# Performance work log

Hardware: AMD Instinct MI355X
Metric: run time of the kernel (lower is better)

## Reference

```python
import jax, jax.numpy as jnp
import numpy as np

B, IC2, N, K = 8, 128, 2048, 32   # x: [B, 2*in_channels, N, k]
C, G = 64, 8                       # out_channels, groups
CPG = C // G                       # channels per group
EPS_BN = 1e-5


def conv1x1(x, w, b=None):
    # 1x1 conv over [B, Cin, N, K] with weight [Cout, Cin]
    y = jnp.einsum('oc,bcnk->bonk', w, x)
    if b is not None:
        y = y + b[None, :, None, None]
    return y


def bn(x, g, beta, m, v):
    # inference-mode BatchNorm2d
    scale = g / jnp.sqrt(v + EPS_BN)
    return x * scale[None, :, None, None] + (beta - m * scale)[None, :, None, None]


def lrelu(x):
    return jax.nn.leaky_relu(x, 0.2)


def setup_inputs() -> dict:
    key = jax.random.key(0)
    ks = jax.random.split(key, 32)
    d = {}
    d['x'] = jax.random.normal(ks[0], (B, IC2, N, K), jnp.float32)
    d['rel_pos'] = jax.random.normal(ks[1], (B, 3, N, K), jnp.float32)
    # pos_net
    d['pos_w1'] = jax.random.normal(ks[2], (C, 3), jnp.float32) * 0.1
    d['pos_bn_g'] = jax.random.uniform(ks[3], (C,), jnp.float32, 0.5, 1.5)
    d['pos_bn_b'] = jax.random.normal(ks[4], (C,), jnp.float32) * 0.1
    d['pos_bn_m'] = jax.random.normal(ks[5], (C,), jnp.float32) * 0.1
    d['pos_bn_v'] = jax.random.uniform(ks[6], (C,), jnp.float32, 0.5, 1.5)
    d['pos_w2'] = jax.random.normal(ks[7], (C, C), jnp.float32) * 0.1
    d['pos_b2'] = jax.random.normal(ks[8], (C,), jnp.float32) * 0.1
    # pe_proj
    d['pe_w'] = jax.random.normal(ks[9], (G, C), jnp.float32) * 0.1
    d['pe_b'] = jax.random.normal(ks[10], (G,), jnp.float32) * 0.1
    # trans (Conv+BN+LeakyReLU)
    d['trans_w'] = jax.random.normal(ks[11], (C, IC2), jnp.float32) * 0.1
    d['trans_bn_g'] = jax.random.uniform(ks[12], (C,), jnp.float32, 0.5, 1.5)
    d['trans_bn_b'] = jax.random.normal(ks[13], (C,), jnp.float32) * 0.1
    d['trans_bn_m'] = jax.random.normal(ks[14], (C,), jnp.float32) * 0.1
    d['trans_bn_v'] = jax.random.uniform(ks[15], (C,), jnp.float32, 0.5, 1.5)
    # gate_net (hidden 16)
    d['gate_w1'] = jax.random.normal(ks[16], (16, IC2), jnp.float32) * 0.1
    d['gate_bn_g'] = jax.random.uniform(ks[17], (16,), jnp.float32, 0.5, 1.5)
    d['gate_bn_b'] = jax.random.normal(ks[18], (16,), jnp.float32) * 0.1
    d['gate_bn_m'] = jax.random.normal(ks[19], (16,), jnp.float32) * 0.1
    d['gate_bn_v'] = jax.random.uniform(ks[20], (16,), jnp.float32, 0.5, 1.5)
    d['gate_w2'] = jax.random.normal(ks[21], (1, 16), jnp.float32) * 0.1
    d['gate_b2'] = jnp.full((1,), 2.0, jnp.float32)  # init.constant_(bias, 2.0)
    # attn_net (hidden C//4 = 16)
    d['attn_w1'] = jax.random.normal(ks[22], (C // 4, IC2), jnp.float32) * 0.1
    d['attn_bn_g'] = jax.random.uniform(ks[23], (C // 4,), jnp.float32, 0.5, 1.5)
    d['attn_bn_b'] = jax.random.normal(ks[24], (C // 4,), jnp.float32) * 0.1
    d['attn_bn_m'] = jax.random.normal(ks[25], (C // 4,), jnp.float32) * 0.1
    d['attn_bn_v'] = jax.random.uniform(ks[26], (C // 4,), jnp.float32, 0.5, 1.5)
    d['attn_w2'] = jax.random.normal(ks[27], (G, C // 4), jnp.float32) * 0.1
    d['attn_b2'] = jax.random.normal(ks[28], (G,), jnp.float32) * 0.1
    return d


def reference(x, rel_pos, pos_w1, pos_bn_g, pos_bn_b, pos_bn_m, pos_bn_v, pos_w2, pos_b2,
              pe_w, pe_b, trans_w, trans_bn_g, trans_bn_b, trans_bn_m, trans_bn_v,
              gate_w1, gate_bn_g, gate_bn_b, gate_bn_m, gate_bn_v, gate_w2, gate_b2,
              attn_w1, attn_bn_g, attn_bn_b, attn_bn_m, attn_bn_v, attn_w2, attn_b2):
    # pos_net: conv -> BN -> LeakyReLU -> conv(bias)
    pos_enc = conv1x1(lrelu(bn(conv1x1(rel_pos, pos_w1), pos_bn_g, pos_bn_b, pos_bn_m, pos_bn_v)),
                      pos_w2, pos_b2)                                    # [B,C,N,K]
    # trans: conv -> BN -> LeakyReLU, plus positional encoding
    trans_feat = lrelu(bn(conv1x1(x, trans_w), trans_bn_g, trans_bn_b, trans_bn_m, trans_bn_v)) + pos_enc
    # gate_net (dropout=identity in eval): -> sigmoid gate [B,1,N,K]
    gate_h = lrelu(bn(conv1x1(x, gate_w1), gate_bn_g, gate_bn_b, gate_bn_m, gate_bn_v))
    gate_map = jax.nn.sigmoid(conv1x1(gate_h, gate_w2, gate_b2))
    # attn_net -> grouped logits [B,G,N,K]
    attn_h = lrelu(bn(conv1x1(x, attn_w1), attn_bn_g, attn_bn_b, attn_bn_m, attn_bn_v))
    attn_logits = conv1x1(attn_h, attn_w2, attn_b2)
    attn_logits = attn_logits + conv1x1(pos_enc, pe_w, pe_b)             # pe_proj
    attn_logits = attn_logits + jnp.log(gate_map + 1e-6)                 # full mode: log-combine gate
    attn_w = jax.nn.softmax(attn_logits, axis=-1)                        # softmax over neighbors k
    attn_w_exp = jnp.repeat(attn_w, CPG, axis=1)                         # repeat_interleave -> [B,C,N,K]
    out_attn = jnp.sum(trans_feat * attn_w_exp, axis=-1)                 # [B,C,N]
    out_max = jnp.max(trans_feat * gate_map, axis=-1)                    # [B,C,N]
    return out_attn + out_max
```

## Files before the change

kernel.cpp:

```cpp
#include <hip/hip_runtime.h>


typedef __attribute__((ext_vector_type(8))) short bf16x8;
typedef __attribute__((ext_vector_type(4))) float f32x4;

#define EPS_BN 1e-5f

__device__ __forceinline__ unsigned pk2(float a, float b){
  unsigned ua = __float_as_uint(a) + 0x8000u;
  unsigned ub = __float_as_uint(b) + 0x8000u;
  return __builtin_amdgcn_perm(ub, ua, 0x07060302);
}
__device__ __forceinline__ short f2bf(float a){
  unsigned u = __float_as_uint(a);
  u += 0x7FFFu + ((u >> 16) & 1u);
  return (short)(u >> 16);
}
__device__ __forceinline__ float lrelu(float v){ return fmaxf(v, 0.2f*v); }

__device__ __forceinline__ void st8(short* dst, float4 a, float4 b){
  *(uint2*)(dst)     = make_uint2(pk2(a.x,a.y), pk2(a.z,a.w));
  *(uint2*)(dst + 4) = make_uint2(pk2(b.x,b.y), pk2(b.z,b.w));
}
__device__ __forceinline__ bf16x8 ld8(const short* p){
  union { bf16x8 v; uint2 q[2]; } w;
  w.q[0] = *(const uint2*)(p);
  w.q[1] = *(const uint2*)(p + 4);
  return w.v;
}

template<int N>
__device__ __forceinline__ float ror16(float x){
  return __int_as_float(__builtin_amdgcn_mov_dpp(__float_as_int(x), 0x120+N, 0xF, 0xF, false));
}
__device__ __forceinline__ float rsum16(float v){
  v += ror16<1>(v); v += ror16<2>(v); v += ror16<4>(v); v += ror16<8>(v); return v;
}
__device__ __forceinline__ float rmax16(float v){
  v = fmaxf(v, ror16<1>(v)); v = fmaxf(v, ror16<2>(v));
  v = fmaxf(v, ror16<4>(v)); v = fmaxf(v, ror16<8>(v)); return v;
}

#define MFMA16(a,b,c) __builtin_amdgcn_mfma_f32_16x16x32_bf16((a),(b),(c),0,0,0)

__global__ __launch_bounds__(256, 2)
void gsl_fused(const float* __restrict__ x,       const float* __restrict__ rel_pos,
               const float* __restrict__ pos_w1,  const float* __restrict__ pos_g,
               const float* __restrict__ pos_bb,  const float* __restrict__ pos_m,
               const float* __restrict__ pos_v,   const float* __restrict__ pos_w2,
               const float* __restrict__ pos_b2,  const float* __restrict__ pe_w,
               const float* __restrict__ pe_b,    const float* __restrict__ trans_w,
               const float* __restrict__ tr_g,    const float* __restrict__ tr_bb,
               const float* __restrict__ tr_m,    const float* __restrict__ tr_v,
               const float* __restrict__ gate_w1, const float* __restrict__ ga_g,
               const float* __restrict__ ga_bb,   const float* __restrict__ ga_m,
               const float* __restrict__ ga_v,    const float* __restrict__ gate_w2,
               const float* __restrict__ gate_b2, const float* __restrict__ attn_w1,
               const float* __restrict__ at_g,    const float* __restrict__ at_bb,
               const float* __restrict__ at_m,    const float* __restrict__ at_v,
               const float* __restrict__ attn_w2, const float* __restrict__ attn_b2,
               float* __restrict__ out)
{
  __shared__ __align__(16) char smem[70784];
  short* xbuf  = (short*)smem;
  short* wmain = (short*)(smem + 33792);
  short* wpos2 = (short*)(smem + 59136);
  float* trQ  = (float*)(smem + 68928);
  float* p1T  = (float*)(smem + 69952);
  float* gaT  = (float*)(smem + 70464);
  float* atT  = (float*)(smem + 70592);
  float* peBt = (float*)(smem + 70720);

  const int tid = threadIdx.x;
  const int wv  = tid >> 6;
  const int l   = tid & 63;
  const int l15 = l & 15, g4 = l >> 4;
  const int bid = blockIdx.x;
  const int b    = bid >> 6;
  const int nblk = (bid & 63) << 5;

  if (tid < 192){
    int r = tid >> 1, c0 = (tid & 1) * 64;
    const float* src = (r < 64) ? (trans_w + r*128)
                     : (r < 80) ? (gate_w1 + (r-64)*128)
                                : (attn_w1 + (r-80)*128);
    src += c0;
    short* dst = wmain + r*132 + c0;
    #pragma unroll
    for (int j = 0; j < 8; ++j)
      st8(dst + 8*j, *(const float4*)(src + 8*j), *(const float4*)(src + 8*j + 4));
  } else {
    int r = tid - 192;
    const float* src = pos_w2 + r*64;
    short* dst = wpos2 + r*68;
    #pragma unroll
    for (int j = 0; j < 8; ++j)
      st8(dst + 8*j, *(const float4*)(src + 8*j), *(const float4*)(src + 8*j + 4));
  }
  if (tid < 64){
    float s = tr_g[tid] * rsqrtf(tr_v[tid] + EPS_BN);
    *(float4*)(trQ + 4*tid) = make_float4(s, tr_bb[tid] - tr_m[tid]*s, pos_b2[tid], 0.f);
    float s2 = pos_g[tid] * rsqrtf(pos_v[tid] + EPS_BN);
    p1T[2*tid] = s2; p1T[2*tid+1] = pos_bb[tid] - pos_m[tid]*s2;
  } else if (tid < 80){
    int c = tid - 64;
    float s = ga_g[c] * rsqrtf(ga_v[c] + EPS_BN);
    gaT[2*c] = s; gaT[2*c+1] = ga_bb[c] - ga_m[c]*s;
  } else if (tid < 96){
    int c = tid - 80;
    float s = at_g[c] * rsqrtf(at_v[c] + EPS_BN);
    atT[2*c] = s; atT[2*c+1] = at_bb[c] - at_m[c]*s;
  } else if (tid < 112){
    int r2 = tid - 96;
    float v = 0.f;
    if (r2 < 8){
      v = pe_b[r2];
      for (int c = 0; c < 64; ++c) v += pe_w[r2*64 + c] * pos_b2[c];
    }
    peBt[r2] = v;
  }
  {
    int o = 2*tid, r = o >> 6, j = o & 63;
    float c0 = 0.f, c1 = 0.f;
    for (int c = 0; c < 64; ++c){
      float a = pe_w[r*64 + c];
      c0 += a * pos_w2[c*64 + j];
      c1 += a * pos_w2[c*64 + j + 1];
    }
    *(unsigned*)(wpos2 + (64 + r)*68 + j) = pk2(c0, c1);
  }

  uint2 pw1p[4];
  #pragma unroll
  for (int m2 = 0; m2 < 4; ++m2){
    uint2 t = make_uint2(0u, 0u);
    if (g4 == 0){
      const float* rp = pos_w1 + (16*m2 + l15)*3;
      t.x = pk2(rp[0], rp[1]);
      t.y = pk2(rp[2], 0.f);
    }
    pw1p[m2] = t;
  }
  bf16x8 gaf;
  {
    bf16x8 t = {0,0,0,0,0,0,0,0};
    #pragma unroll
    for (int j = 0; j < 8; ++j){
      int k = 8*g4 + j;
      float v2 = 0.f;
      if (l15 < 8)       { if (k >= 16) v2 = attn_w2[l15*16 + (k-16)]; }
      else if (l15 == 8) { if (k < 16)  v2 = gate_w2[k]; }
      t[j] = f2bf(v2);
    }
    gaf = t;
  }
  const float gb2v = gate_b2[0];

  __syncthreads();

  float lcr[4];
  #pragma unroll
  for (int r = 0; r < 4; ++r){
    int row = 4*g4 + r;
    lcr[r] = peBt[row] + ((row < 8) ? attn_b2[row] : 0.f);
  }

  const int col0 = 32*wv + l15, col1 = col0 + 16;
  const int lc0 = l15, lc1 = l15 + 16;
  const int lq = l & 7, ld = l >> 3;
  const int colb = 32*wv + 4*lq;
  char*  slice = smem + wv*8448;
  short* h1b   = (short*)slice;
  short* gab   = (short*)(slice + 4352);
  const float* xp0 = x + (((long)(b*128 + 8*ld)) << 16) + colb;
  const float* rpb = rel_pos + (((long)(3*b)) << 16);
  float* outb = out + (((long)(b*64)) << 11) + nblk + wv;

  f32x4 fa[8], fb[8];
  float rc[6] = {0.f,0.f,0.f,0.f,0.f,0.f};
  {
    const long sb0 = (long)nblk * 32;
    #pragma unroll
    for (int j = 0; j < 8; ++j) fa[j] = *(const f32x4*)(xp0 + sb0 + (((long)j) << 16));
    #pragma unroll
    for (int j = 0; j < 8; ++j) fb[j] = *(const f32x4*)(xp0 + sb0 + (((long)(64+j)) << 16));
    if (g4 == 0){
      long sg = sb0 + col0;
      rc[0] = rpb[sg];          rc[1] = rpb[sg + 65536];      rc[2] = rpb[sg + 131072];
      rc[3] = rpb[sg + 16];     rc[4] = rpb[sg + 65536 + 16]; rc[5] = rpb[sg + 131072 + 16];
    }
  }

  for (int it = 0; it < 8; ++it){
    const long sbase = (long)nblk*32 + 128*it;

    #pragma unroll
    for (int i2 = 0; i2 < 4; ++i2){
      short* dst = xbuf + (colb+i2)*132 + 8*ld;
      *(uint2*)(dst)      = make_uint2(pk2(fa[0][i2],fa[1][i2]), pk2(fa[2][i2],fa[3][i2]));
      *(uint2*)(dst + 4)  = make_uint2(pk2(fa[4][i2],fa[5][i2]), pk2(fa[6][i2],fa[7][i2]));
      *(uint2*)(dst + 64) = make_uint2(pk2(fb[0][i2],fb[1][i2]), pk2(fb[2][i2],fb[3][i2]));
      *(uint2*)(dst + 68) = make_uint2(pk2(fb[4][i2],fb[5][i2]), pk2(fb[6][i2],fb[7][i2]));
    }

    const long nsb = sbase + 128;
    if (it < 7){
      #pragma unroll
      for (int j = 0; j < 8; ++j) fa[j] = *(const f32x4*)(xp0 + nsb + (((long)j) << 16));
    }

    f32x4 acc[6][2];
    #pragma unroll
    for (int m = 0; m < 6; ++m){
      f32x4 z = {0.f,0.f,0.f,0.f};
      acc[m][0] = z; acc[m][1] = z;
    }
    #pragma unroll
    for (int ks = 0; ks < 4; ++ks){
      bf16x8 b0 = ld8(xbuf + col0*132 + 32*ks + 8*g4);
      bf16x8 b1 = ld8(xbuf + col1*132 + 32*ks + 8*g4);
      #pragma unroll
      for (int m = 0; m < 6; ++m){
        bf16x8 af = ld8(wmain + (16*m + l15)*132 + 32*ks + 8*g4);
        acc[m][0] = MFMA16(af, b0, acc[m][0]);
        acc[m][1] = MFMA16(af, b1, acc[m][1]);
      }
    }

    if (it < 7){
      #pragma unroll
      for (int j = 0; j < 8; ++j) fb[j] = *(const f32x4*)(xp0 + nsb + (((long)(64+j)) << 16));
    }

    {
      bf16x8 rf0 = {0,0,0,0,0,0,0,0}, rf1 = {0,0,0,0,0,0,0,0};
      if (g4 == 0){
        union { bf16x8 v; unsigned u[4]; } t0, t1;
        t0.u[0] = pk2(rc[0], rc[1]); t0.u[1] = pk2(rc[2], 0.f); t0.u[2] = 0u; t0.u[3] = 0u;
        t1.u[0] = pk2(rc[3], rc[4]); t1.u[1] = pk2(rc[5], 0.f); t1.u[2] = 0u; t1.u[3] = 0u;
        rf0 = t0.v; rf1 = t1.v;
      }
      #pragma unroll
      for (int m2 = 0; m2 < 4; ++m2){
        union { bf16x8 v; unsigned u[4]; } aw;
        aw.u[0] = pw1p[m2].x; aw.u[1] = pw1p[m2].y; aw.u[2] = 0u; aw.u[3] = 0u;
        f32x4 z = {0.f,0.f,0.f,0.f};
        f32x4 d0 = MFMA16(aw.v, rf0, z);
        f32x4 d1 = MFMA16(aw.v, rf1, z);
        int cb2 = 16*m2 + 4*g4;
        float2 t0 = *(const float2*)(p1T + 2*(cb2+0));
        float2 t1 = *(const float2*)(p1T + 2*(cb2+1));
        float2 t2 = *(const float2*)(p1T + 2*(cb2+2));
        float2 t3 = *(const float2*)(p1T + 2*(cb2+3));
        float h0 = lrelu(t0.x*d0[0]+t0.y), h1v = lrelu(t1.x*d0[1]+t1.y);
        float h2 = lrelu(t2.x*d0[2]+t2.y), h3 = lrelu(t3.x*d0[3]+t3.y);
        *(uint2*)(h1b + lc0*68 + cb2) = make_uint2(pk2(h0,h1v), pk2(h2,h3));
        h0 = lrelu(t0.x*d1[0]+t0.y); h1v = lrelu(t1.x*d1[1]+t1.y);
        h2 = lrelu(t2.x*d1[2]+t2.y); h3 = lrelu(t3.x*d1[3]+t3.y);
        *(uint2*)(h1b + lc1*68 + cb2) = make_uint2(pk2(h0,h1v), pk2(h2,h3));
      }
    }
    if (g4 == 0 && it < 7){
      long sg = nsb + col0;
      rc[0] = rpb[sg];          rc[1] = rpb[sg + 65536];      rc[2] = rpb[sg + 131072];
      rc[3] = rpb[sg + 16];     rc[4] = rpb[sg + 65536 + 16]; rc[5] = rpb[sg + 131072 + 16];
    }

    #pragma unroll
    for (int m = 0; m < 4; ++m)
      #pragma unroll
      for (int r = 0; r < 4; ++r){
        float4 tq = *(const float4*)(trQ + 4*(16*m + 4*g4 + r));
        acc[m][0][r] = lrelu(tq.x*acc[m][0][r] + tq.y) + tq.z;
        acc[m][1][r] = lrelu(tq.x*acc[m][1][r] + tq.y) + tq.z;
      }

    f32x4 pac4[2];
    {
      f32x4 z = {0.f,0.f,0.f,0.f};
      pac4[0] = z; pac4[1] = z;
    }
    #pragma unroll
    for (int ks = 0; ks < 2; ++ks){
      bf16x8 h0 = ld8(h1b + lc0*68 + 32*ks + 8*g4);
      bf16x8 h1v = ld8(h1b + lc1*68 + 32*ks + 8*g4);
      #pragma unroll
      for (int m2 = 0; m2 < 4; ++m2){
        bf16x8 af = ld8(wpos2 + (16*m2 + l15)*68 + 32*ks + 8*g4);
        acc[m2][0] = MFMA16(af, h0, acc[m2][0]);
        acc[m2][1] = MFMA16(af, h1v, acc[m2][1]);
      }
      bf16x8 af4 = ld8(wpos2 + (64 + l15)*68 + 32*ks + 8*g4);
      pac4[0] = MFMA16(af4, h0, pac4[0]);
      pac4[1] = MFMA16(af4, h1v, pac4[1]);
    }

    {
      int hc = 4*g4;
      float2 g0p = *(const float2*)(gaT + 2*(hc+0));
      float2 g1p = *(const float2*)(gaT + 2*(hc+1));
      float2 g2p = *(const float2*)(gaT + 2*(hc+2));
      float2 g3p = *(const float2*)(gaT + 2*(hc+3));
      float2 a0p = *(const float2*)(atT + 2*(hc+0));
      float2 a1p = *(const float2*)(atT + 2*(hc+1));
      float2 a2p = *(const float2*)(atT + 2*(hc+2));
      float2 a3p = *(const float2*)(atT + 2*(hc+3));
      #pragma unroll
      for (int ct = 0; ct < 2; ++ct){
        int lc = (ct == 0) ? lc0 : lc1;
        float q0 = lrelu(g0p.x*acc[4][ct][0] + g0p.y), q1 = lrelu(g1p.x*acc[4][ct][1] + g1p.y);
        float q2 = lrelu(g2p.x*acc[4][ct][2] + g2p.y), q3 = lrelu(g3p.x*acc[4][ct][3] + g3p.y);
        *(uint2*)(gab + lc*36 + hc) = make_uint2(pk2(q0,q1), pk2(q2,q3));
        float a0 = lrelu(a0p.x*acc[5][ct][0] + a0p.y), a1 = lrelu(a1p.x*acc[5][ct][1] + a1p.y);
        float a2 = lrelu(a2p.x*acc[5][ct][2] + a2p.y), a3 = lrelu(a3p.x*acc[5][ct][3] + a3p.y);
        *(uint2*)(gab + lc*36 + 16 + hc) = make_uint2(pk2(a0,a1), pk2(a2,a3));
      }
    }

    f32x4 gac0 = {0.f,0.f,0.f,0.f}, gac1 = gac0;
    {
      bf16x8 g0 = ld8(gab + lc0*36 + 8*g4);
      bf16x8 g1 = ld8(gab + lc1*36 + 8*g4);
      gac0 = MFMA16(gaf, g0, gac0);
      gac1 = MFMA16(gaf, g1, gac1);
    }

    float gv0 = __shfl(gac0[0], 32 + l15, 64);
    float gv1 = __shfl(gac1[0], 32 + l15, 64);
    float gm0 = 1.f/(1.f + __expf(-(gv0 + gb2v)));
    float gm1 = 1.f/(1.f + __expf(-(gv1 + gb2v)));
    float lg0 = __logf(gm0 + 1e-6f), lg1 = __logf(gm1 + 1e-6f);

    float wg0[4], wg1[4];
    #pragma unroll
    for (int r = 0; r < 4; ++r){
      float t0 = gac0[r] + pac4[0][r] + lcr[r] + lg0;
      float t1 = gac1[r] + pac4[1][r] + lcr[r] + lg1;
      float mx = rmax16(fmaxf(t0, t1));
      float e0 = __expf(t0 - mx), e1 = __expf(t1 - mx);
      float inv = 1.f / rsum16(e0 + e1);
      wg0[r] = e0 * inv; wg1[r] = e1 * inv;
    }
    float wf0[8], wf1[8];
    #pragma unroll
    for (int gg = 0; gg < 8; ++gg){
      int src = 16*(gg >> 2) + l15;
      wf0[gg] = __shfl(wg0[gg & 3], src, 64);
      wf1[gg] = __shfl(wg1[gg & 3], src, 64);
    }
    const bool hi = (g4 >= 2);
    #pragma unroll
    for (int m = 0; m < 4; ++m){
      float w0 = hi ? wf0[2*m+1] : wf0[2*m];
      float w1 = hi ? wf1[2*m+1] : wf1[2*m];
      #pragma unroll
      for (int r = 0; r < 4; ++r){
        float sA = rsum16(acc[m][0][r]*w0 + acc[m][1][r]*w1);
        float sM = rmax16(fmaxf(acc[m][0][r]*gm0, acc[m][1][r]*gm1));
        if (l15 == 0)
          outb[(((long)(16*m + 4*g4 + r)) << 11) + 4*it] = sA + sM;
      }
    }
  }
}

extern "C" void kernel_launch(void* const* d_in, const int* in_sizes, int n_in,
                              void* d_out, int out_size, void* d_ws, size_t ws_size,
                              hipStream_t stream){
  (void)in_sizes; (void)n_in; (void)out_size; (void)d_ws; (void)ws_size;
  gsl_fused<<<dim3(512), dim3(256), 0, stream>>>(
    (const float*)d_in[0],  (const float*)d_in[1],  (const float*)d_in[2],
    (const float*)d_in[3],  (const float*)d_in[4],  (const float*)d_in[5],
    (const float*)d_in[6],  (const float*)d_in[7],  (const float*)d_in[8],
    (const float*)d_in[9],  (const float*)d_in[10], (const float*)d_in[11],
    (const float*)d_in[12], (const float*)d_in[13], (const float*)d_in[14],
    (const float*)d_in[15], (const float*)d_in[16], (const float*)d_in[17],
    (const float*)d_in[18], (const float*)d_in[19], (const float*)d_in[20],
    (const float*)d_in[21], (const float*)d_in[22], (const float*)d_in[23],
    (const float*)d_in[24], (const float*)d_in[25], (const float*)d_in[26],
    (const float*)d_in[27], (const float*)d_in[28], (const float*)d_in[29],
    (float*)d_out);
}
```

Baseline: 75.44 us.

## Hoist pe_w·pos_w2 fold to prep kernel and use transpose-reduce for outputs

Moves the per-block folding of pe_w with pos_w2 and pe_b with pos_b2 into a single-block prep kernel that writes to workspace. The main kernel now only loads those results, which removes a 64-iteration dot-product loop from every block's prologue. The barrier is moved after the first global prefetch so those loads overlap the setup. The epilogue replaces 32 separate 16-lane DPP reductions, each written by one lane, with a butterfly transpose-reduce so every lane ends up owning one output channel and stores it. The cost is an extra kernel launch and a dependency on workspace.

Result: faster. 70.02 us (median of 2 runs) (-7.2%).

```diff
diff --git a/kernel.cpp b/kernel.cpp
--- a/kernel.cpp
+++ b/kernel.cpp
@@ -43,13 +43,30 @@
 
 #define MFMA16(a,b,c) __builtin_amdgcn_mfma_f32_16x16x32_bf16((a),(b),(c),0,0,0)
 
+__global__ void gsl_prep(const float* __restrict__ pos_w2, const float* __restrict__ pe_w,
+                         const float* __restrict__ pe_b,   const float* __restrict__ pos_b2,
+                         float* __restrict__ ws){
+  int t = threadIdx.x;
+  int r = t >> 6, j = t & 63;
+  float s = 0.f;
+  for (int c = 0; c < 64; ++c) s += pe_w[r*64 + c] * pos_w2[c*64 + j];
+  ws[t] = s;
+  if (t < 16){
+    float v = 0.f;
+    if (t < 8){
+      v = pe_b[t];
+      for (int c = 0; c < 64; ++c) v += pe_w[t*64 + c] * pos_b2[c];
+    }
+    ws[512 + t] = v;
+  }
+}
+
 __global__ __launch_bounds__(256, 2)
 void gsl_fused(const float* __restrict__ x,       const float* __restrict__ rel_pos,
                const float* __restrict__ pos_w1,  const float* __restrict__ pos_g,
                const float* __restrict__ pos_bb,  const float* __restrict__ pos_m,
                const float* __restrict__ pos_v,   const float* __restrict__ pos_w2,
-               const float* __restrict__ pos_b2,  const float* __restrict__ pe_w,
-               const float* __restrict__ pe_b,    const float* __restrict__ trans_w,
+               const float* __restrict__ pos_b2,  const float* __restrict__ trans_w,
                const float* __restrict__ tr_g,    const float* __restrict__ tr_bb,
                const float* __restrict__ tr_m,    const float* __restrict__ tr_v,
                const float* __restrict__ gate_w1, const float* __restrict__ ga_g,
@@ -59,7 +76,7 @@
                const float* __restrict__ at_g,    const float* __restrict__ at_bb,
                const float* __restrict__ at_m,    const float* __restrict__ at_v,
                const float* __restrict__ attn_w2, const float* __restrict__ attn_b2,
-               float* __restrict__ out)
+               const float* __restrict__ ws,      float* __restrict__ out)
 {
   __shared__ __align__(16) char smem[70784];
   short* xbuf  = (short*)smem;
@@ -69,7 +86,6 @@
   float* p1T  = (float*)(smem + 69952);
   float* gaT  = (float*)(smem + 70464);
   float* atT  = (float*)(smem + 70592);
-  float* peBt = (float*)(smem + 70720);
 
   const int tid = threadIdx.x;
   const int wv  = tid >> 6;
@@ -95,6 +111,14 @@
     short* dst = wpos2 + r*68;
     #pragma unroll
     for (int j = 0; j < 8; ++j)
+      st8(dst + 8*j, *(const float4*)(src + 8*j), *(const float4*)(src + 8*j + 4));
+  }
+  if (tid < 16){
+    int r = tid >> 1, c0 = (tid & 1) * 32;
+    const float* src = ws + r*64 + c0;
+    short* dst = wpos2 + (64 + r)*68 + c0;
+    #pragma unroll
+    for (int j = 0; j < 4; ++j)
       st8(dst + 8*j, *(const float4*)(src + 8*j), *(const float4*)(src + 8*j + 4));
   }
   if (tid < 64){
@@ -110,24 +134,6 @@
     int c = tid - 80;
     float s = at_g[c] * rsqrtf(at_v[c] + EPS_BN);
     atT[2*c] = s; atT[2*c+1] = at_bb[c] - at_m[c]*s;
-  } else if (tid < 112){
-    int r2 = tid - 96;
-    float v = 0.f;
-    if (r2 < 8){
-      v = pe_b[r2];
-      for (int c = 0; c < 64; ++c) v += pe_w[r2*64 + c] * pos_b2[c];
-    }
-    peBt[r2] = v;
-  }
-  {
-    int o = 2*tid, r = o >> 6, j = o & 63;
-    float c0 = 0.f, c1 = 0.f;
-    for (int c = 0; c < 64; ++c){
-      float a = pe_w[r*64 + c];
-      c0 += a * pos_w2[c*64 + j];
-      c1 += a * pos_w2[c*64 + j + 1];
-    }
-    *(unsigned*)(wpos2 + (64 + r)*68 + j) = pk2(c0, c1);
   }
 
   uint2 pw1p[4];
@@ -155,14 +161,11 @@
     gaf = t;
   }
   const float gb2v = gate_b2[0];
-
-  __syncthreads();
-
   float lcr[4];
   #pragma unroll
   for (int r = 0; r < 4; ++r){
     int row = 4*g4 + r;
-    lcr[r] = peBt[row] + ((row < 8) ? attn_b2[row] : 0.f);
+    lcr[r] = ws[512 + row] + ((row < 8) ? attn_b2[row] : 0.f);
   }
 
   const int col0 = 32*wv + l15, col1 = col0 + 16;
@@ -174,7 +177,8 @@
   short* gab   = (short*)(slice + 4352);
   const float* xp0 = x + (((long)(b*128 + 8*ld)) << 16) + colb;
   const float* rpb = rel_pos + (((long)(3*b)) << 16);
-  float* outb = out + (((long)(b*64)) << 11) + nblk + wv;
+  const int och = 16*(l15 >> 2) + 4*g4 + (l15 & 3);
+  float* outb = out + (((long)(b*64 + och)) << 11) + nblk + wv;
 
   f32x4 fa[8], fb[8];
   float rc[6] = {0.f,0.f,0.f,0.f,0.f,0.f};
@@ -190,6 +194,8 @@
       rc[3] = rpb[sg + 16];     rc[4] = rpb[sg + 65536 + 16]; rc[5] = rpb[sg + 131072 + 16];
     }
   }
+
+  __syncthreads();
 
   for (int it = 0; it < 8; ++it){
     const long sbase = (long)nblk*32 + 128*it;
@@ -341,43 +347,58 @@
       float inv = 1.f / rsum16(e0 + e1);
       wg0[r] = e0 * inv; wg1[r] = e1 * inv;
     }
-    float wf0[8], wf1[8];
-    #pragma unroll
-    for (int gg = 0; gg < 8; ++gg){
-      int src = 16*(gg >> 2) + l15;
-      wf0[gg] = __shfl(wg0[gg & 3], src, 64);
-      wf1[gg] = __shfl(wg1[gg & 3], src, 64);
-    }
+
+    float vA[16], vM[16];
     const bool hi = (g4 >= 2);
     #pragma unroll
     for (int m = 0; m < 4; ++m){
-      float w0 = hi ? wf0[2*m+1] : wf0[2*m];
-      float w1 = hi ? wf1[2*m+1] : wf1[2*m];
+      int src = 16*(m >> 1) + l15;
+      float a0 = __shfl(wg0[(2*m) & 3],   src, 64);
+      float b0 = __shfl(wg0[(2*m+1) & 3], src, 64);
+      float a1 = __shfl(wg1[(2*m) & 3],   src, 64);
+      float b1 = __shfl(wg1[(2*m+1) & 3], src, 64);
+      float w0 = hi ? b0 : a0;
+      float w1 = hi ? b1 : a1;
       #pragma unroll
       for (int r = 0; r < 4; ++r){
-        float sA = rsum16(acc[m][0][r]*w0 + acc[m][1][r]*w1);
-        float sM = rmax16(fmaxf(acc[m][0][r]*gm0, acc[m][1][r]*gm1));
-        if (l15 == 0)
-          outb[(((long)(16*m + 4*g4 + r)) << 11) + 4*it] = sA + sM;
-      }
-    }
+        vA[4*m+r] = acc[m][0][r]*w0 + acc[m][1][r]*w1;
+        vM[4*m+r] = fmaxf(acc[m][0][r]*gm0, acc[m][1][r]*gm1);
+      }
+    }
+    #pragma unroll
+    for (int s = 0; s < 4; ++s){
+      const int mm = 8 >> s;
+      const bool up = (l15 & mm) != 0;
+      #pragma unroll
+      for (int k2 = 0; k2 < mm; ++k2){
+        float sendA = up ? vA[k2] : vA[k2 + mm];
+        float keepA = up ? vA[k2 + mm] : vA[k2];
+        vA[k2] = keepA + __shfl_xor(sendA, mm, 64);
+        float sendM = up ? vM[k2] : vM[k2 + mm];
+        float keepM = up ? vM[k2 + mm] : vM[k2];
+        vM[k2] = fmaxf(keepM, __shfl_xor(sendM, mm, 64));
+      }
+    }
+    outb[4*it] = vA[0] + vM[0];
   }
 }
 
 extern "C" void kernel_launch(void* const* d_in, const int* in_sizes, int n_in,
                               void* d_out, int out_size, void* d_ws, size_t ws_size,
                               hipStream_t stream){
-  (void)in_sizes; (void)n_in; (void)out_size; (void)d_ws; (void)ws_size;
+  (void)in_sizes; (void)n_in; (void)out_size; (void)ws_size;
+  gsl_prep<<<dim3(1), dim3(512), 0, stream>>>(
+    (const float*)d_in[7], (const float*)d_in[9], (const float*)d_in[10],
+    (const float*)d_in[8], (float*)d_ws);
   gsl_fused<<<dim3(512), dim3(256), 0, stream>>>(
     (const float*)d_in[0],  (const float*)d_in[1],  (const float*)d_in[2],
     (const float*)d_in[3],  (const float*)d_in[4],  (const float*)d_in[5],
     (const float*)d_in[6],  (const float*)d_in[7],  (const float*)d_in[8],
-    (const float*)d_in[9],  (const float*)d_in[10], (const float*)d_in[11],
-    (const float*)d_in[12], (const float*)d_in[13], (const float*)d_in[14],
-    (const float*)d_in[15], (const float*)d_in[16], (const float*)d_in[17],
-    (const float*)d_in[18], (const float*)d_in[19], (const float*)d_in[20],
-    (const float*)d_in[21], (const float*)d_in[22], (const float*)d_in[23],
-    (const float*)d_in[24], (const float*)d_in[25], (const float*)d_in[26],
-    (const float*)d_in[27], (const float*)d_in[28], (const float*)d_in[29],
-    (float*)d_out);
-}
+    (const float*)d_in[11], (const float*)d_in[12], (const float*)d_in[13],
+    (const float*)d_in[14], (const float*)d_in[15], (const float*)d_in[16],
+    (const float*)d_in[17], (const float*)d_in[18], (const float*)d_in[19],
+    (const float*)d_in[20], (const float*)d_in[21], (const float*)d_in[22],
+    (const float*)d_in[23], (const float*)d_in[24], (const float*)d_in[25],
+    (const float*)d_in[26], (const float*)d_in[27], (const float*)d_in[28],
+    (const float*)d_in[29], (const float*)d_ws, (float*)d_out);
+}
```
